# Optimization experiments

Hardware: AMD Instinct MI355X
Metric: run time of the kernel (lower is better)

Reference implementation:

```python
import jax, jax.numpy as jnp
import numpy as np

D_MODEL = 1024
NHEAD = 16
HEAD_DIM = D_MODEL // NHEAD
B, S = 8, 1024
NEG = -1e9  # finite stand-in for -inf (same softmax result, grad-safe)


def setup_inputs() -> dict:
    key = jax.random.key(0)
    ks = jax.random.split(key, 12)
    sc = 1.0 / np.sqrt(D_MODEL)
    inp = {
        "q": jax.random.normal(ks[0], (B, S, D_MODEL), jnp.float32),
        "k": jax.random.normal(ks[1], (B, S, D_MODEL), jnp.float32),
        "v": jax.random.normal(ks[2], (B, S, D_MODEL), jnp.float32),
        "padding_mask": jax.random.bernoulli(ks[3], 0.1, (B, S)),
        "causal_mask": jnp.where(jnp.tril(jnp.ones((S, S), bool)), 0.0, NEG).astype(jnp.float32),
        "wq": jax.random.normal(ks[4], (D_MODEL, D_MODEL), jnp.float32) * sc,
        "bq": jax.random.normal(ks[5], (D_MODEL,), jnp.float32) * sc,
        "wk": jax.random.normal(ks[6], (D_MODEL, D_MODEL), jnp.float32) * sc,
        "wv": jax.random.normal(ks[7], (D_MODEL, D_MODEL), jnp.float32) * sc,
        "bv": jax.random.normal(ks[8], (D_MODEL,), jnp.float32) * sc,
        "wo": jax.random.normal(ks[9], (D_MODEL, D_MODEL), jnp.float32) * sc,
        "bo": jax.random.normal(ks[10], (D_MODEL,), jnp.float32) * sc,
    }
    return inp


def reference(q, k, v, padding_mask, causal_mask, wq, bq, wk, wv, bv, wo, bo):
    b = q.shape[0]
    # projections (torch Linear: x @ W.T + b); k_linear has no bias
    qp = q @ wq.T + bq
    kp = k @ wk.T
    vp = v @ wv.T + bv
    # [B, S, H, Dh] -> [B, H, S, Dh]
    qh = qp.reshape(b, -1, NHEAD, HEAD_DIM).transpose(0, 2, 1, 3)
    kh = kp.reshape(b, -1, NHEAD, HEAD_DIM).transpose(0, 2, 1, 3)
    vh = vp.reshape(b, -1, NHEAD, HEAD_DIM).transpose(0, 2, 1, 3)
    scores = jnp.einsum("bhqd,bhkd->bhqk", qh, kh) / np.sqrt(HEAD_DIM).astype(np.float32)
    scores = jnp.where(padding_mask[:, None, None, :], NEG, scores)
    scores = scores + causal_mask[None, None, :, :]
    attn = jax.nn.softmax(scores, axis=-1)
    out = jnp.einsum("bhqk,bhkd->bhqd", attn, vh)
    out = out.transpose(0, 2, 1, 3).reshape(b, -1, D_MODEL)
    return out @ wo.T + bo
```

## Files before the change

### kernel.cpp

```cpp
#include <hip/hip_runtime.h>
#include <hip/hip_bf16.h>
#include <cstdint>
#include <math.h>


typedef __bf16 bf16_t;
typedef __bf16 bf16x8 __attribute__((ext_vector_type(8)));
typedef __bf16 bf16x4 __attribute__((ext_vector_type(4)));
typedef float  f32x4  __attribute__((ext_vector_type(4)));

#define MFMA16(a, b, c) __builtin_amdgcn_mfma_f32_16x16x32_bf16((a), (b), (c), 0, 0, 0)
#define NEGV (-1e9f)

__device__ __forceinline__ void gl_lds16(const void* gp, void* lp) {
  __builtin_amdgcn_global_load_lds(
      (__attribute__((address_space(1))) void*)(gp),
      (__attribute__((address_space(3))) void*)(lp), 16, 0, 0);
}

__device__ __forceinline__ unsigned int pk2(float lo, float hi) {
  unsigned short a = __builtin_bit_cast(unsigned short, (bf16_t)lo);
  unsigned short b = __builtin_bit_cast(unsigned short, (bf16_t)hi);
  return (unsigned int)a | ((unsigned int)b << 16);
}

__device__ __forceinline__ void cvt_body(const float* __restrict__ in,
                                         bf16_t* __restrict__ out, int i) {
  const float4* p = reinterpret_cast<const float4*>(in) + (size_t)i * 2;
  float4 a = p[0], b = p[1];
  bf16x8 r = {(bf16_t)a.x, (bf16_t)a.y, (bf16_t)a.z, (bf16_t)a.w,
              (bf16_t)b.x, (bf16_t)b.y, (bf16_t)b.z, (bf16_t)b.w};
  *reinterpret_cast<bf16x8*>(out + (size_t)i * 8) = r;
}

__global__ __launch_bounds__(256) void cvt_all(
    const float* __restrict__ q, const float* __restrict__ k, const float* __restrict__ v,
    const float* __restrict__ wq, const float* __restrict__ wk,
    const float* __restrict__ wv, const float* __restrict__ wo,
    bf16_t* __restrict__ oq, bf16_t* __restrict__ ok, bf16_t* __restrict__ ov,
    bf16_t* __restrict__ owq, bf16_t* __restrict__ owk,
    bf16_t* __restrict__ owv, bf16_t* __restrict__ owo) {
  const int bid = (int)blockIdx.x;
  if (bid < 12288) {
    const int s = bid >> 12;
    const int i = (bid & 4095) * 256 + (int)threadIdx.x;
    cvt_body(s == 0 ? q : (s == 1 ? k : v),
             s == 0 ? oq : (s == 1 ? ok : ov), i);
  } else {
    const int r = bid - 12288;
    const int s = r >> 9;
    const int i = (r & 511) * 256 + (int)threadIdx.x;
    cvt_body(s == 0 ? wq : (s == 1 ? wk : (s == 2 ? wv : wo)),
             s == 0 ? owq : (s == 1 ? owk : (s == 2 ? owv : owo)), i);
  }
}

__device__ __forceinline__ void panel_decode(int r, int& bx, int& by) {
  const int t8 = r >> 3;
  bx = t8 & 7;
  by = ((t8 >> 3) << 3) | (r & 7);
}

__global__ __launch_bounds__(256) void gemm_qkv(const bf16_t* __restrict__ qbf,
                                                const bf16_t* __restrict__ kbf,
                                                const bf16_t* __restrict__ vbf,
                                                const bf16_t* __restrict__ wqb,
                                                const bf16_t* __restrict__ wkb,
                                                const bf16_t* __restrict__ wvb,
                                                const float* __restrict__ bq,
                                                const float* __restrict__ bv,
                                                bf16_t* __restrict__ qp,
                                                bf16_t* __restrict__ kp,
                                                bf16_t* __restrict__ vtw) {
  __shared__ bf16_t smem[6][128 * 32];
  const int z = blockIdx.y;
  const bf16_t* A = z == 0 ? qbf : (z == 1 ? kbf : vbf);
  const bf16_t* W = z == 0 ? wqb : (z == 1 ? wkb : wvb);
  const int t = threadIdx.x;
  const int w = t >> 6, l = t & 63, lr = l & 15, lg = l >> 4;
  int bx, by;
  panel_decode((int)blockIdx.x, bx, by);
  const int m0 = by * 128, n0 = bx * 128;
  const int wm = (w >> 1) * 64, wn = (w & 1) * 64;
  const int K = 1024, N = 1024;

  f32x4 acc[4][4] = {};
  const int swsrc = ((t & 3) ^ ((t >> 3) & 3)) * 8;
  const bf16_t* Ag = A + (size_t)(m0 + (t >> 2)) * K + swsrc;
  const bf16_t* Wg = W + (size_t)(n0 + (t >> 2)) * K + swsrc;

  auto stage = [&](int buf, int tile) {
    const int kt = tile * 32;
    gl_lds16(Ag + kt,                  (char*)(smem[buf])     + t * 16);
    gl_lds16(Ag + kt + (size_t)64 * K, (char*)(smem[buf])     + 4096 + t * 16);
    gl_lds16(Wg + kt,                  (char*)(smem[3 + buf]) + t * 16);
    gl_lds16(Wg + kt + (size_t)64 * K, (char*)(smem[3 + buf]) + 4096 + t * 16);
  };

  stage(0, 0);
  stage(1, 1);

  const int cofs = ((lg ^ ((lr >> 1) & 3)) << 4);
  for (int it = 0; it < 32; ++it) {
    if (it < 31) asm volatile("s_waitcnt vmcnt(4)" ::: "memory");
    else         asm volatile("s_waitcnt vmcnt(0)" ::: "memory");
    __builtin_amdgcn_s_barrier();
    if (it + 2 < 32) stage((it + 2) % 3, it + 2);

    const char* AsB = (const char*)(smem[it % 3]);
    const char* BsB = (const char*)(smem[3 + it % 3]);
    bf16x8 af[4], bfr[4];
#pragma unroll
    for (int mt = 0; mt < 4; mt++)
      af[mt] = *reinterpret_cast<const bf16x8*>(AsB + (wm + mt * 16 + lr) * 64 + cofs);
#pragma unroll
    for (int nt = 0; nt < 4; nt++)
      bfr[nt] = *reinterpret_cast<const bf16x8*>(BsB + (wn + nt * 16 + lr) * 64 + cofs);
#pragma unroll
    for (int mt = 0; mt < 4; mt++)
#pragma unroll
      for (int nt = 0; nt < 4; nt++)
        acc[mt][nt] = MFMA16(af[mt], bfr[nt], acc[mt][nt]);
  }

  if (z != 2) {
    bf16_t* outp = (z == 0) ? qp : kp;
    const float sc = (z == 0) ? 0.125f : 1.0f;
#pragma unroll
    for (int nt = 0; nt < 4; nt++) {
      const int col = n0 + wn + nt * 16 + lr;
      const float bb = (z == 0) ? bq[col] : 0.0f;
#pragma unroll
      for (int mt = 0; mt < 4; mt++)
#pragma unroll
        for (int i = 0; i < 4; i++) {
          const int row = m0 + wm + mt * 16 + lg * 4 + i;
          outp[(size_t)row * N + col] = (bf16_t)((acc[mt][nt][i] + bb) * sc);
        }
    }
  } else {
    __syncthreads();
    char* T = (char*)smem;
#pragma unroll
    for (int nt = 0; nt < 4; nt++) {
      const int col_l = wn + nt * 16 + lr;
      const float bb = bv[n0 + col_l];
#pragma unroll
      for (int mt = 0; mt < 4; mt++)
#pragma unroll
        for (int i = 0; i < 4; i++) {
          const int row_l = wm + mt * 16 + lg * 4 + i;
          *(bf16_t*)(T + col_l * 256 + ((row_l * 2) ^ ((col_l & 7) << 4))) =
              (bf16_t)(acc[mt][nt][i] + bb);
        }
    }
    __syncthreads();
    const int b = m0 >> 10, s0 = m0 & 1023;
    const int c_l = t >> 1, half = t & 1;
    bf16_t* dst = vtw + (size_t)(b * 1024 + n0 + c_l) * 1024 + s0 + half * 64;
    const char* Trow = T + c_l * 256;
    const int sw = c_l & 7;
#pragma unroll
    for (int jj = 0; jj < 8; jj++) {
      const int lc = half * 8 + jj;
      bf16x8 vv = *reinterpret_cast<const bf16x8*>(Trow + ((lc ^ sw) << 4));
      *reinterpret_cast<bf16x8*>(dst + jj * 8) = vv;
    }
  }
}

__global__ __launch_bounds__(256) void gemm_out(const bf16_t* __restrict__ A,
                                                const bf16_t* __restrict__ W,
                                                const float* __restrict__ bias,
                                                float* __restrict__ outp) {
  __shared__ bf16_t smem[6][128 * 32];
  const int t = threadIdx.x;
  const int w = t >> 6, l = t & 63, lr = l & 15, lg = l >> 4;
  int bx, by;
  panel_decode((int)blockIdx.x, bx, by);
  const int m0 = by * 128, n0 = bx * 128;
  const int wm = (w >> 1) * 64, wn = (w & 1) * 64;
  const int K = 1024, N = 1024;

  f32x4 acc[4][4] = {};
  const int swsrc = ((t & 3) ^ ((t >> 3) & 3)) * 8;
  const bf16_t* Ag = A + (size_t)(m0 + (t >> 2)) * K + swsrc;
  const bf16_t* Wg = W + (size_t)(n0 + (t >> 2)) * K + swsrc;

  auto stage = [&](int buf, int tile) {
    const int kt = tile * 32;
    gl_lds16(Ag + kt,                  (char*)(smem[buf])     + t * 16);
    gl_lds16(Ag + kt + (size_t)64 * K, (char*)(smem[buf])     + 4096 + t * 16);
    gl_lds16(Wg + kt,                  (char*)(smem[3 + buf]) + t * 16);
    gl_lds16(Wg + kt + (size_t)64 * K, (char*)(smem[3 + buf]) + 4096 + t * 16);
  };

  stage(0, 0);
  stage(1, 1);

  const int cofs = ((lg ^ ((lr >> 1) & 3)) << 4);
  for (int it = 0; it < 32; ++it) {
    if (it < 31) asm volatile("s_waitcnt vmcnt(4)" ::: "memory");
    else         asm volatile("s_waitcnt vmcnt(0)" ::: "memory");
    __builtin_amdgcn_s_barrier();
    if (it + 2 < 32) stage((it + 2) % 3, it + 2);

    const char* AsB = (const char*)(smem[it % 3]);
    const char* BsB = (const char*)(smem[3 + it % 3]);
    bf16x8 af[4], bfr[4];
#pragma unroll
    for (int mt = 0; mt < 4; mt++)
      af[mt] = *reinterpret_cast<const bf16x8*>(AsB + (wm + mt * 16 + lr) * 64 + cofs);
#pragma unroll
    for (int nt = 0; nt < 4; nt++)
      bfr[nt] = *reinterpret_cast<const bf16x8*>(BsB + (wn + nt * 16 + lr) * 64 + cofs);
#pragma unroll
    for (int mt = 0; mt < 4; mt++)
#pragma unroll
      for (int nt = 0; nt < 4; nt++)
        acc[mt][nt] = MFMA16(af[mt], bfr[nt], acc[mt][nt]);
  }

#pragma unroll
  for (int nt = 0; nt < 4; nt++) {
    const int col = n0 + wn + nt * 16 + lr;
    const float bb = bias[col];
#pragma unroll
    for (int mt = 0; mt < 4; mt++)
#pragma unroll
      for (int i = 0; i < 4; i++) {
        const int row = m0 + wm + mt * 16 + lg * 4 + i;
        outp[(size_t)row * N + col] = acc[mt][nt][i] + bb;
      }
  }
}

__device__ __forceinline__ void pack_bfly(const f32x4 (&s)[4], int lg,
                                          bf16x8& pbv0, bf16x8& pbv1) {
  unsigned int u[4][2], sh[4][2];
#pragma unroll
  for (int nt = 0; nt < 4; nt++) {
    u[nt][0] = pk2(s[nt][0], s[nt][1]);
    u[nt][1] = pk2(s[nt][2], s[nt][3]);
  }
#pragma unroll
  for (int nt = 0; nt < 4; nt++) {
    sh[nt][0] = (unsigned int)__shfl_xor((int)u[nt][0], 16, 64);
    sh[nt][1] = (unsigned int)__shfl_xor((int)u[nt][1], 16, 64);
  }
  const bool ev = (lg & 1) == 0;
  unsigned int Y[8];
  Y[0] = ev ? u[0][0] : sh[1][0];  Y[1] = ev ? u[0][1] : sh[1][1];
  Y[2] = ev ? u[2][0] : sh[3][0];  Y[3] = ev ? u[2][1] : sh[3][1];
  Y[4] = ev ? sh[0][0] : u[1][0];  Y[5] = ev ? sh[0][1] : u[1][1];
  Y[6] = ev ? sh[2][0] : u[3][0];  Y[7] = ev ? sh[2][1] : u[3][1];
  const bool mid = (lg == 1) || (lg == 2);
#pragma unroll
  for (int j = 0; j < 8; j++) {
    const unsigned int z = (unsigned int)__shfl_xor((int)Y[j], 48, 64);
    Y[j] = mid ? z : Y[j];
  }
  union U8 { unsigned int u[4]; bf16x8 v; };
  U8 p0, p1;
  p0.u[0] = Y[0]; p0.u[1] = Y[1]; p0.u[2] = Y[4]; p0.u[3] = Y[5];
  p1.u[0] = Y[2]; p1.u[1] = Y[3]; p1.u[2] = Y[6]; p1.u[3] = Y[7];
  pbv0 = p0.v;
  pbv1 = p1.v;
}

__global__ __launch_bounds__(512, 8) void attn_fused(const bf16_t* __restrict__ qp,
                                                     const bf16_t* __restrict__ kp,
                                                     const bf16_t* __restrict__ vt,
                                                     const int* __restrict__ pad,
                                                     bf16_t* __restrict__ outp) {
  __shared__ bf16_t Ks[2][64 * 64];
  __shared__ bf16_t Vts[2][64 * 64];
  __shared__ int padI[1024];
  __shared__ int sfl[8], sfh[8];
  const int t = threadIdx.x, w = t >> 6, l = t & 63, lr = l & 15, lg = l >> 4;
  const int L = (int)blockIdx.x;
  const int bh = (L & 7) + ((L >> 6) << 3);
  const int j = (L >> 3) & 7;
  const int b = bh >> 4, h = bh & 15;
  const int lo = j, hi = 15 - j;

  const int srow = t >> 3, sc = t & 7;
  const int gc = sc ^ (srow & 7);
  const bf16_t* kgb = kp + (size_t)(b * 1024 + srow) * 1024 + h * 64 + gc * 8;
  const bf16_t* vgb = vt + (size_t)(bh * 64 + srow) * 1024 + gc * 8;

  auto stage = [&](int bufi, int k0s) {
    gl_lds16(kgb + (size_t)k0s * 1024, (char*)(Ks[bufi]) + t * 16);
    gl_lds16(vgb + k0s,                (char*)(Vts[bufi]) + t * 16);
  };

  bool unl = false, unh = false;
  for (int jj = t; jj <= hi * 64; jj += 512) {
    const bool u = (pad[b * 1024 + jj] == 0);
    unh |= u;
    unl |= (u && (jj <= lo * 64));
  }
  const bool al = __any(unl), ah = __any(unh);
  if (l == 0) { sfl[w] = al ? 1 : 0; sfh[w] = ah ? 1 : 0; }

  stage(0, 0);
  if (t < 256) gl_lds16(pad + b * 1024 + t * 4, (char*)padI + t * 16);

  const int mytile = (w < 4) ? hi : lo;
  const int qrow_l = mytile * 64 + (w & 3) * 16 + lr;
  const int base16 = mytile * 64 + (w & 3) * 16;
  const bf16_t* qg = qp + (size_t)(b * 1024 + qrow_l) * 1024 + h * 64 + lg * 8;
  const bf16x8 qa0 = *reinterpret_cast<const bf16x8*>(qg);
  const bf16x8 qa1 = *reinterpret_cast<const bf16x8*>(qg + 32);

  __syncthreads();
  int ul = 0, uh = 0;
#pragma unroll
  for (int i = 0; i < 8; i++) { ul |= sfl[i]; uh |= sfh[i]; }
  const bool mydeg = (w < 4) ? (uh == 0) : (ul == 0);
  const int ktEnd = (ul == 0) ? 16 : (hi + 1);

  f32x4 o[4] = {};
  float m_ = -INFINITY, ld_ = 0.0f;

  for (int kt = 0; kt < ktEnd; ++kt) {
    const int cur = kt & 1;
    if (kt + 1 < ktEnd) {
      stage(cur ^ 1, (kt + 1) * 64);
      asm volatile("s_waitcnt vmcnt(2)" ::: "memory");
    } else {
      asm volatile("s_waitcnt vmcnt(0)" ::: "memory");
    }
    __builtin_amdgcn_s_barrier();

    if (kt <= mytile || mydeg) {
      const char* Kb = (const char*)(Ks[cur]);
      const char* Vb = (const char*)(Vts[cur]);
      const int k0 = kt * 64;

      f32x4 s[4] = {};
#pragma unroll
      for (int nt = 0; nt < 4; nt++) {
        const int row = nt * 16 + lr;
        const int sw = (row & 7) << 4;
        bf16x8 kb0 = *reinterpret_cast<const bf16x8*>(Kb + row * 128 + ((lg * 16) ^ sw));
        bf16x8 kb1 = *reinterpret_cast<const bf16x8*>(Kb + row * 128 + ((lg * 16 + 64) ^ sw));
        s[nt] = MFMA16(kb0, qa0, s[nt]);
        s[nt] = MFMA16(kb1, qa1, s[nt]);
      }

      const bool nc = (k0 + 63 > base16);
#pragma unroll
      for (int nt = 0; nt < 4; nt++) {
        const int kc4 = k0 + nt * 16 + lg * 4;
        const int4 pd = *reinterpret_cast<const int4*>(&padI[kc4]);
        const int pdv[4] = {pd.x, pd.y, pd.z, pd.w};
#pragma unroll
        for (int i = 0; i < 4; i++) {
          float v = s[nt][i];
          if (pdv[i]) v = NEGV;
          if (nc && (kc4 + i > qrow_l)) v += NEGV;
          s[nt][i] = v;
        }
      }

      float mx = s[0][0];
#pragma unroll
      for (int nt = 0; nt < 4; nt++)
#pragma unroll
        for (int i = 0; i < 4; i++) mx = fmaxf(mx, s[nt][i]);
      mx = fmaxf(mx, __shfl_xor(mx, 16, 64));
      mx = fmaxf(mx, __shfl_xor(mx, 32, 64));

      if (!__all(mx <= m_ - 88.0f)) {
        if (!__all(mx <= m_ + 8.0f)) {
          const float mn = fmaxf(m_, mx);
          const float scl = __expf(m_ - mn);
          m_ = mn;
          ld_ *= scl;
#pragma unroll
          for (int nt = 0; nt < 4; nt++) o[nt] *= scl;
        }
        float a = 0.0f;
#pragma unroll
        for (int nt = 0; nt < 4; nt++)
#pragma unroll
          for (int i = 0; i < 4; i++) {
            const float p = __expf(s[nt][i] - m_);
            s[nt][i] = p;
            a += p;
          }
        a += __shfl_xor(a, 16, 64);
        a += __shfl_xor(a, 32, 64);
        ld_ += a;

        bf16x8 pb0, pb1;
        pack_bfly(s, lg, pb0, pb1);

#pragma unroll
        for (int nt = 0; nt < 4; nt++) {
          const int vrow = nt * 16 + lr;
          const int vsw = (vrow & 7) << 4;
          bf16x8 vf0 = *reinterpret_cast<const bf16x8*>(Vb + vrow * 128 + ((lg * 16) ^ vsw));
          bf16x8 vf1 = *reinterpret_cast<const bf16x8*>(Vb + vrow * 128 + ((64 + lg * 16) ^ vsw));
          o[nt] = MFMA16(vf0, pb0, o[nt]);
          o[nt] = MFMA16(vf1, pb1, o[nt]);
        }
      }
    }
    __builtin_amdgcn_s_barrier();
  }

  const float rinv = 1.0f / ld_;
#pragma unroll
  for (int nt = 0; nt < 4; nt++) {
    bf16x4 r = {(bf16_t)(o[nt][0] * rinv), (bf16_t)(o[nt][1] * rinv),
                (bf16_t)(o[nt][2] * rinv), (bf16_t)(o[nt][3] * rinv)};
    *reinterpret_cast<bf16x4*>(outp + (size_t)(b * 1024 + qrow_l) * 1024 + h * 64 + nt * 16 + lg * 4) = r;
  }
}

extern "C" void kernel_launch(void* const* d_in, const int* in_sizes, int n_in,
                              void* d_out, int out_size, void* d_ws, size_t ws_size,
                              hipStream_t stream) {
  const float* q   = (const float*)d_in[0];
  const float* k   = (const float*)d_in[1];
  const float* v   = (const float*)d_in[2];
  const int*   pad = (const int*)d_in[3];
  const float* wq  = (const float*)d_in[5];
  const float* bq  = (const float*)d_in[6];
  const float* wk  = (const float*)d_in[7];
  const float* wv  = (const float*)d_in[8];
  const float* bv  = (const float*)d_in[9];
  const float* wo  = (const float*)d_in[10];
  const float* bo  = (const float*)d_in[11];

  char* ws = (char*)d_ws;
  const size_t MiB = 1024 * 1024;
  bf16_t* qbf = (bf16_t*)(ws + 0 * MiB);
  bf16_t* kbf = (bf16_t*)(ws + 16 * MiB);
  bf16_t* vbf = (bf16_t*)(ws + 32 * MiB);
  bf16_t* qp  = (bf16_t*)(ws + 48 * MiB);
  bf16_t* kp  = (bf16_t*)(ws + 64 * MiB);
  bf16_t* vtw = (bf16_t*)(ws + 80 * MiB);
  bf16_t* wqb = (bf16_t*)(ws + 96 * MiB);
  bf16_t* wkb = (bf16_t*)(ws + 98 * MiB);
  bf16_t* wvb = (bf16_t*)(ws + 100 * MiB);
  bf16_t* wob = (bf16_t*)(ws + 102 * MiB);
  bf16_t* attnO = qbf;

  cvt_all<<<14336, 256, 0, stream>>>(q, k, v, wq, wk, wv, wo,
                                     qbf, kbf, vbf, wqb, wkb, wvb, wob);

  gemm_qkv<<<dim3(512, 3), 256, 0, stream>>>(qbf, kbf, vbf, wqb, wkb, wvb, bq, bv, qp, kp, vtw);

  attn_fused<<<1024, 512, 0, stream>>>(qp, kp, vtw, pad, attnO);

  gemm_out<<<512, 256, 0, stream>>>(attnO, wob, bo, (float*)d_out);
}
```

Before: 187.4 us.

## Rewrite QKV projection GEMM with 256x256 tiles and 8-wave ping-pong pipeline

```diff
diff --git a/kernel.cpp b/kernel.cpp
--- a/kernel.cpp
+++ b/kernel.cpp
@@ -16,6 +16,12 @@
   __builtin_amdgcn_global_load_lds(
       (__attribute__((address_space(1))) void*)(gp),
       (__attribute__((address_space(3))) void*)(lp), 16, 0, 0);
+}
+
+__device__ __forceinline__ void bar() {
+  asm volatile("" ::: "memory");
+  __builtin_amdgcn_s_barrier();
+  asm volatile("" ::: "memory");
 }
 
 __device__ __forceinline__ unsigned int pk2(float lo, float hi) {
@@ -55,13 +61,7 @@
   }
 }
 
-__device__ __forceinline__ void panel_decode(int r, int& bx, int& by) {
-  const int t8 = r >> 3;
-  bx = t8 & 7;
-  by = ((t8 >> 3) << 3) | (r & 7);
-}
-
-__global__ __launch_bounds__(256) void gemm_qkv(const bf16_t* __restrict__ qbf,
+__global__ __launch_bounds__(512) void gemm_qkv(const bf16_t* __restrict__ qbf,
                                                 const bf16_t* __restrict__ kbf,
                                                 const bf16_t* __restrict__ vbf,
                                                 const bf16_t* __restrict__ wqb,
@@ -72,55 +72,128 @@
                                                 bf16_t* __restrict__ qp,
                                                 bf16_t* __restrict__ kp,
                                                 bf16_t* __restrict__ vtw) {
-  __shared__ bf16_t smem[6][128 * 32];
-  const int z = blockIdx.y;
+  __shared__ __align__(16) char lds[131072];
+  const int bid = (int)blockIdx.x;
+  const int z = bid >> 7;
+  const int r = bid & 127;
+  const int p = ((r >> 5) << 3) | (r & 7);
+  const int ntile = (r >> 3) & 3;
   const bf16_t* A = z == 0 ? qbf : (z == 1 ? kbf : vbf);
   const bf16_t* W = z == 0 ? wqb : (z == 1 ? wkb : wvb);
   const int t = threadIdx.x;
   const int w = t >> 6, l = t & 63, lr = l & 15, lg = l >> 4;
-  int bx, by;
-  panel_decode((int)blockIdx.x, bx, by);
-  const int m0 = by * 128, n0 = bx * 128;
-  const int wm = (w >> 1) * 64, wn = (w & 1) * 64;
+  const int wr = w >> 2, wc = w & 3;
+  const int m0 = p * 256, n0 = ntile * 256;
   const int K = 1024, N = 1024;
 
-  f32x4 acc[4][4] = {};
-  const int swsrc = ((t & 3) ^ ((t >> 3) & 3)) * 8;
-  const bf16_t* Ag = A + (size_t)(m0 + (t >> 2)) * K + swsrc;
-  const bf16_t* Wg = W + (size_t)(n0 + (t >> 2)) * K + swsrc;
-
-  auto stage = [&](int buf, int tile) {
-    const int kt = tile * 32;
-    gl_lds16(Ag + kt,                  (char*)(smem[buf])     + t * 16);
-    gl_lds16(Ag + kt + (size_t)64 * K, (char*)(smem[buf])     + 4096 + t * 16);
-    gl_lds16(Wg + kt,                  (char*)(smem[3 + buf]) + t * 16);
-    gl_lds16(Wg + kt + (size_t)64 * K, (char*)(smem[3 + buf]) + 4096 + t * 16);
+  const int gc = (t & 7) ^ ((t >> 3) & 7);
+  const bf16_t* Ag = A + (size_t)(m0 + (t >> 3)) * K + gc * 8;
+  const bf16_t* Wg = W + (size_t)(n0 + (t >> 3)) * K + gc * 8;
+
+  auto stageA = [&](int buf, int tile, int half) {
+    char* dst = lds + buf * 65536 + half * 16384 + t * 16;
+    const size_t kt = (size_t)tile * 64;
+    gl_lds16(Ag + (size_t)(half * 128) * K + kt,      dst);
+    gl_lds16(Ag + (size_t)(half * 128 + 64) * K + kt, dst + 8192);
   };
-
-  stage(0, 0);
-  stage(1, 1);
-
-  const int cofs = ((lg ^ ((lr >> 1) & 3)) << 4);
-  for (int it = 0; it < 32; ++it) {
-    if (it < 31) asm volatile("s_waitcnt vmcnt(4)" ::: "memory");
-    else         asm volatile("s_waitcnt vmcnt(0)" ::: "memory");
-    __builtin_amdgcn_s_barrier();
-    if (it + 2 < 32) stage((it + 2) % 3, it + 2);
-
-    const char* AsB = (const char*)(smem[it % 3]);
-    const char* BsB = (const char*)(smem[3 + it % 3]);
-    bf16x8 af[4], bfr[4];
-#pragma unroll
-    for (int mt = 0; mt < 4; mt++)
-      af[mt] = *reinterpret_cast<const bf16x8*>(AsB + (wm + mt * 16 + lr) * 64 + cofs);
-#pragma unroll
-    for (int nt = 0; nt < 4; nt++)
-      bfr[nt] = *reinterpret_cast<const bf16x8*>(BsB + (wn + nt * 16 + lr) * 64 + cofs);
-#pragma unroll
-    for (int mt = 0; mt < 4; mt++)
-#pragma unroll
-      for (int nt = 0; nt < 4; nt++)
-        acc[mt][nt] = MFMA16(af[mt], bfr[nt], acc[mt][nt]);
+  auto stageB = [&](int buf, int tile, int half) {
+    char* dst = lds + buf * 65536 + 32768 + half * 16384 + t * 16;
+    const size_t kt = (size_t)tile * 64;
+    gl_lds16(Wg + (size_t)(half * 128) * K + kt,      dst);
+    gl_lds16(Wg + (size_t)(half * 128 + 64) * K + kt, dst + 8192);
+  };
+
+  stageA(0, 0, 0); stageA(0, 0, 1); stageB(0, 0, 0); stageB(0, 0, 1);
+  stageB(1, 1, 0); stageB(1, 1, 1); stageA(1, 1, 0);
+  asm volatile("s_waitcnt vmcnt(6)" ::: "memory");
+  bar();
+
+  f32x4 acc[8][4] = {};
+  const int xorv = (lr & 7) << 4;
+  const int k0o = lg * 16, k1o = 64 + lg * 16;
+
+  for (int T = 0; T < 16; ++T) {
+    const int cur = T & 1;
+    const char* Ab = lds + cur * 65536;
+    const char* Bb = Ab + 32768;
+
+    bf16x8 a0[4][2], a1[4][2], b0[2][2], b1[2][2];
+#pragma unroll
+    for (int mt = 0; mt < 4; mt++) {
+      const int row = wr * 128 + mt * 16 + lr;
+      a0[mt][0] = *(const bf16x8*)(Ab + row * 128 + (k0o ^ xorv));
+      a0[mt][1] = *(const bf16x8*)(Ab + row * 128 + (k1o ^ xorv));
+    }
+#pragma unroll
+    for (int nt = 0; nt < 2; nt++) {
+      const int row = wc * 64 + nt * 16 + lr;
+      b0[nt][0] = *(const bf16x8*)(Bb + row * 128 + (k0o ^ xorv));
+      b0[nt][1] = *(const bf16x8*)(Bb + row * 128 + (k1o ^ xorv));
+    }
+    if (T + 1 < 16) stageA(cur ^ 1, T + 1, 1);
+    bar();
+    asm volatile("s_waitcnt lgkmcnt(0)" ::: "memory");
+    __builtin_amdgcn_s_setprio(1);
+#pragma unroll
+    for (int mt = 0; mt < 4; mt++)
+#pragma unroll
+      for (int nt = 0; nt < 2; nt++) {
+        acc[mt][nt] = MFMA16(a0[mt][0], b0[nt][0], acc[mt][nt]);
+        acc[mt][nt] = MFMA16(a0[mt][1], b0[nt][1], acc[mt][nt]);
+      }
+    __builtin_amdgcn_s_setprio(0);
+    bar();
+#pragma unroll
+    for (int nt = 0; nt < 2; nt++) {
+      const int row = wc * 64 + (nt + 2) * 16 + lr;
+      b1[nt][0] = *(const bf16x8*)(Bb + row * 128 + (k0o ^ xorv));
+      b1[nt][1] = *(const bf16x8*)(Bb + row * 128 + (k1o ^ xorv));
+    }
+    bar();
+    asm volatile("s_waitcnt lgkmcnt(0)" ::: "memory");
+    __builtin_amdgcn_s_setprio(1);
+#pragma unroll
+    for (int mt = 0; mt < 4; mt++)
+#pragma unroll
+      for (int nt = 0; nt < 2; nt++) {
+        acc[mt][nt + 2] = MFMA16(a0[mt][0], b1[nt][0], acc[mt][nt + 2]);
+        acc[mt][nt + 2] = MFMA16(a0[mt][1], b1[nt][1], acc[mt][nt + 2]);
+      }
+    __builtin_amdgcn_s_setprio(0);
+    bar();
+#pragma unroll
+    for (int mt = 0; mt < 4; mt++) {
+      const int row = wr * 128 + (mt + 4) * 16 + lr;
+      a1[mt][0] = *(const bf16x8*)(Ab + row * 128 + (k0o ^ xorv));
+      a1[mt][1] = *(const bf16x8*)(Ab + row * 128 + (k1o ^ xorv));
+    }
+    if (T + 2 < 16) stageB(cur, T + 2, 0);
+    bar();
+    asm volatile("s_waitcnt lgkmcnt(0)" ::: "memory");
+    __builtin_amdgcn_s_setprio(1);
+#pragma unroll
+    for (int mt = 0; mt < 4; mt++)
+#pragma unroll
+      for (int nt = 0; nt < 2; nt++) {
+        acc[mt + 4][nt + 2] = MFMA16(a1[mt][0], b1[nt][0], acc[mt + 4][nt + 2]);
+        acc[mt + 4][nt + 2] = MFMA16(a1[mt][1], b1[nt][1], acc[mt + 4][nt + 2]);
+      }
+    __builtin_amdgcn_s_setprio(0);
+    bar();
+    if (T + 2 < 16) { stageB(cur, T + 2, 1); stageA(cur, T + 2, 0); }
+    if (T < 14)       asm volatile("s_waitcnt vmcnt(6)" ::: "memory");
+    else if (T == 14) asm volatile("s_waitcnt vmcnt(0)" ::: "memory");
+    bar();
+    __builtin_amdgcn_s_setprio(1);
+#pragma unroll
+    for (int mt = 0; mt < 4; mt++)
+#pragma unroll
+      for (int nt = 0; nt < 2; nt++) {
+        acc[mt + 4][nt] = MFMA16(a1[mt][0], b0[nt][0], acc[mt + 4][nt]);
+        acc[mt + 4][nt] = MFMA16(a1[mt][1], b0[nt][1], acc[mt + 4][nt]);
+      }
+    __builtin_amdgcn_s_setprio(0);
+    bar();
   }
 
   if (z != 2) {
@@ -128,45 +201,50 @@
     const float sc = (z == 0) ? 0.125f : 1.0f;
 #pragma unroll
     for (int nt = 0; nt < 4; nt++) {
-      const int col = n0 + wn + nt * 16 + lr;
+      const int col = n0 + wc * 64 + nt * 16 + lr;
       const float bb = (z == 0) ? bq[col] : 0.0f;
 #pragma unroll
-      for (int mt = 0; mt < 4; mt++)
+      for (int mt = 0; mt < 8; mt++)
 #pragma unroll
         for (int i = 0; i < 4; i++) {
-          const int row = m0 + wm + mt * 16 + lg * 4 + i;
+          const int row = m0 + wr * 128 + mt * 16 + lg * 4 + i;
           outp[(size_t)row * N + col] = (bf16_t)((acc[mt][nt][i] + bb) * sc);
         }
     }
   } else {
     __syncthreads();
-    char* T = (char*)smem;
+    char* Tl = lds;
 #pragma unroll
     for (int nt = 0; nt < 4; nt++) {
-      const int col_l = wn + nt * 16 + lr;
+      const int col_l = wc * 64 + nt * 16 + lr;
       const float bb = bv[n0 + col_l];
 #pragma unroll
-      for (int mt = 0; mt < 4; mt++)
+      for (int mt = 0; mt < 8; mt++)
 #pragma unroll
         for (int i = 0; i < 4; i++) {
-          const int row_l = wm + mt * 16 + lg * 4 + i;
-          *(bf16_t*)(T + col_l * 256 + ((row_l * 2) ^ ((col_l & 7) << 4))) =
+          const int row_l = wr * 128 + mt * 16 + lg * 4 + i;
+          *(bf16_t*)(Tl + col_l * 512 + ((row_l * 2) ^ ((col_l & 7) << 4))) =
               (bf16_t)(acc[mt][nt][i] + bb);
         }
     }
     __syncthreads();
     const int b = m0 >> 10, s0 = m0 & 1023;
-    const int c_l = t >> 1, half = t & 1;
-    bf16_t* dst = vtw + (size_t)(b * 1024 + n0 + c_l) * 1024 + s0 + half * 64;
-    const char* Trow = T + c_l * 256;
-    const int sw = c_l & 7;
-#pragma unroll
-    for (int jj = 0; jj < 8; jj++) {
-      const int lc = half * 8 + jj;
-      bf16x8 vv = *reinterpret_cast<const bf16x8*>(Trow + ((lc ^ sw) << 4));
-      *reinterpret_cast<bf16x8*>(dst + jj * 8) = vv;
-    }
-  }
+    const int c_l = t >> 1, hf = t & 1;
+    bf16_t* dst = vtw + (size_t)(b * 1024 + n0 + c_l) * 1024 + s0 + hf * 128;
+    const char* Trow = Tl + c_l * 512;
+    const int sw2 = (c_l & 7) << 4;
+#pragma unroll
+    for (int jj = 0; jj < 16; jj++) {
+      bf16x8 vv = *(const bf16x8*)(Trow + ((((hf * 16 + jj) << 4)) ^ sw2));
+      *(bf16x8*)(dst + jj * 8) = vv;
+    }
+  }
+}
+
+__device__ __forceinline__ void panel_decode(int r, int& bx, int& by) {
+  const int t8 = r >> 3;
+  bx = t8 & 7;
+  by = ((t8 >> 3) << 3) | (r & 7);
 }
 
 __global__ __launch_bounds__(256) void gemm_out(const bf16_t* __restrict__ A,
@@ -187,8 +265,7 @@
   const bf16_t* Ag = A + (size_t)(m0 + (t >> 2)) * K + swsrc;
   const bf16_t* Wg = W + (size_t)(n0 + (t >> 2)) * K + swsrc;
 
-  auto stage = [&](int buf, int tile) {
-    const int kt = tile * 32;
+  auto stage = [&](int buf, int kt) {
     gl_lds16(Ag + kt,                  (char*)(smem[buf])     + t * 16);
     gl_lds16(Ag + kt + (size_t)64 * K, (char*)(smem[buf])     + 4096 + t * 16);
     gl_lds16(Wg + kt,                  (char*)(smem[3 + buf]) + t * 16);
@@ -196,14 +273,15 @@
   };
 
   stage(0, 0);
-  stage(1, 1);
+  stage(1, 32);
 
   const int cofs = ((lg ^ ((lr >> 1) & 3)) << 4);
   for (int it = 0; it < 32; ++it) {
     if (it < 31) asm volatile("s_waitcnt vmcnt(4)" ::: "memory");
     else         asm volatile("s_waitcnt vmcnt(0)" ::: "memory");
     __builtin_amdgcn_s_barrier();
-    if (it + 2 < 32) stage((it + 2) % 3, it + 2);
+    asm volatile("" ::: "memory");
+    if (it + 2 < 32) stage((it + 2) % 3, (it + 2) * 32);
 
     const char* AsB = (const char*)(smem[it % 3]);
     const char* BsB = (const char*)(smem[3 + it % 3]);
@@ -414,9 +492,9 @@
   const float rinv = 1.0f / ld_;
 #pragma unroll
   for (int nt = 0; nt < 4; nt++) {
-    bf16x4 r = {(bf16_t)(o[nt][0] * rinv), (bf16_t)(o[nt][1] * rinv),
-                (bf16_t)(o[nt][2] * rinv), (bf16_t)(o[nt][3] * rinv)};
-    *reinterpret_cast<bf16x4*>(outp + (size_t)(b * 1024 + qrow_l) * 1024 + h * 64 + nt * 16 + lg * 4) = r;
+    bf16x4 rr = {(bf16_t)(o[nt][0] * rinv), (bf16_t)(o[nt][1] * rinv),
+                 (bf16_t)(o[nt][2] * rinv), (bf16_t)(o[nt][3] * rinv)};
+    *reinterpret_cast<bf16x4*>(outp + (size_t)(b * 1024 + qrow_l) * 1024 + h * 64 + nt * 16 + lg * 4) = rr;
   }
 }
 
@@ -452,7 +530,7 @@
   cvt_all<<<14336, 256, 0, stream>>>(q, k, v, wq, wk, wv, wo,
                                      qbf, kbf, vbf, wqb, wkb, wvb, wob);
 
-  gemm_qkv<<<dim3(512, 3), 256, 0, stream>>>(qbf, kbf, vbf, wqb, wkb, wvb, bq, bv, qp, kp, vtw);
+  gemm_qkv<<<384, 512, 0, stream>>>(qbf, kbf, vbf, wqb, wkb, wvb, bq, bv, qp, kp, vtw);
 
   attn_fused<<<1024, 512, 0, stream>>>(qp, kp, vtw, pad, attnO);
 
```

Result: no change. 187.4 us (+0.0%).

## Restructure projection GEMMs to 256x128 tiles with 8 waves and split-phase pipeline

Applied to the files above, without the earlier changes.

```diff
diff --git a/kernel.cpp b/kernel.cpp
--- a/kernel.cpp
+++ b/kernel.cpp
@@ -16,6 +16,12 @@
   __builtin_amdgcn_global_load_lds(
       (__attribute__((address_space(1))) void*)(gp),
       (__attribute__((address_space(3))) void*)(lp), 16, 0, 0);
+}
+
+__device__ __forceinline__ void bar() {
+  asm volatile("" ::: "memory");
+  __builtin_amdgcn_s_barrier();
+  asm volatile("" ::: "memory");
 }
 
 __device__ __forceinline__ unsigned int pk2(float lo, float hi) {
@@ -55,13 +61,83 @@
   }
 }
 
-__device__ __forceinline__ void panel_decode(int r, int& bx, int& by) {
-  const int t8 = r >> 3;
-  bx = t8 & 7;
-  by = ((t8 >> 3) << 3) | (r & 7);
-}
-
-__global__ __launch_bounds__(256) void gemm_qkv(const bf16_t* __restrict__ qbf,
+
+#define GEMM_KLOOP(Ag, Wg, lds, acc, lr, lg, wr, wc)                          \
+  auto stageA = [&](int buf, int tile) {                                      \
+    char* dst = lds + buf * 32768 + t * 16;                                   \
+    const size_t kt = (size_t)tile * 64;                                      \
+    gl_lds16(Ag + kt,                    dst);                                \
+    gl_lds16(Ag + kt + (size_t)64 * K,   dst + 8192);                         \
+    gl_lds16(Ag + kt + (size_t)128 * K,  dst + 16384);                        \
+    gl_lds16(Ag + kt + (size_t)192 * K,  dst + 24576);                        \
+  };                                                                          \
+  auto stageB = [&](int buf, int tile) {                                      \
+    char* dst = lds + 98304 + buf * 16384 + t * 16;                           \
+    const size_t kt = (size_t)tile * 64;                                      \
+    gl_lds16(Wg + kt,                    dst);                                \
+    gl_lds16(Wg + kt + (size_t)64 * K,   dst + 8192);                         \
+  };                                                                          \
+  stageA(0, 0); stageB(0, 0); stageA(1, 1); stageB(1, 1);                     \
+  asm volatile("s_waitcnt vmcnt(6)" ::: "memory");   \
+  bar();                                                      \
+  const int xorv = (lr & 7) << 4;                                             \
+  const int k0o = lg * 16, k1o = 64 + lg * 16;                                \
+  for (int T = 0; T < 16; ++T) {                                              \
+    const int cur = T % 3;                                                    \
+    const char* Ab = lds + cur * 32768;                                       \
+    const char* Bb = lds + 98304 + cur * 16384;                               \
+    bf16x8 af[4][2], b0[2][2], b1[2][2];                                      \
+                                \
+    _Pragma("unroll")                                                         \
+    for (int mt = 0; mt < 4; mt++) {                                          \
+      const int row = wr * 64 + mt * 16 + lr;                                 \
+      af[mt][0] = *(const bf16x8*)(Ab + row * 128 + (k0o ^ xorv));            \
+      af[mt][1] = *(const bf16x8*)(Ab + row * 128 + (k1o ^ xorv));            \
+    }                                                                         \
+    _Pragma("unroll")                                                         \
+    for (int nt = 0; nt < 2; nt++) {                                          \
+      const int row = wc * 64 + nt * 16 + lr;                                 \
+      b0[nt][0] = *(const bf16x8*)(Bb + row * 128 + (k0o ^ xorv));            \
+      b0[nt][1] = *(const bf16x8*)(Bb + row * 128 + (k1o ^ xorv));            \
+    }                                                                         \
+    if (T + 2 < 16) stageA((T + 2) % 3, T + 2);                               \
+    bar();                                                                    \
+    asm volatile("s_waitcnt lgkmcnt(0)" ::: "memory");                        \
+    __builtin_amdgcn_s_setprio(1);                                            \
+    _Pragma("unroll")                                                         \
+    for (int mt = 0; mt < 4; mt++)                                            \
+      _Pragma("unroll")                                                       \
+      for (int nt = 0; nt < 2; nt++) {                                        \
+        acc[mt][nt] = MFMA16(af[mt][0], b0[nt][0], acc[mt][nt]);              \
+        acc[mt][nt] = MFMA16(af[mt][1], b0[nt][1], acc[mt][nt]);              \
+      }                                                                       \
+    __builtin_amdgcn_s_setprio(0);                                            \
+    bar();                                                                    \
+            \
+    _Pragma("unroll")                                                         \
+    for (int nt = 0; nt < 2; nt++) {                                          \
+      const int row = wc * 64 + (nt + 2) * 16 + lr;                           \
+      b1[nt][0] = *(const bf16x8*)(Bb + row * 128 + (k0o ^ xorv));            \
+      b1[nt][1] = *(const bf16x8*)(Bb + row * 128 + (k1o ^ xorv));            \
+    }                                                                         \
+    if (T + 2 < 16) stageB((T + 2) % 3, T + 2);                               \
+    if (T < 14)       asm volatile("s_waitcnt vmcnt(6)" ::: "memory");        \
+    else if (T == 14) asm volatile("s_waitcnt vmcnt(0)" ::: "memory");        \
+    bar();                                     \
+    asm volatile("s_waitcnt lgkmcnt(0)" ::: "memory");                        \
+    __builtin_amdgcn_s_setprio(1);                                            \
+    _Pragma("unroll")                                                         \
+    for (int mt = 0; mt < 4; mt++)                                            \
+      _Pragma("unroll")                                                       \
+      for (int nt = 0; nt < 2; nt++) {                                        \
+        acc[mt][nt + 2] = MFMA16(af[mt][0], b1[nt][0], acc[mt][nt + 2]);      \
+        acc[mt][nt + 2] = MFMA16(af[mt][1], b1[nt][1], acc[mt][nt + 2]);      \
+      }                                                                       \
+    __builtin_amdgcn_s_setprio(0);                                            \
+    bar();                                                                    \
+  }
+
+__global__ __launch_bounds__(512) void gemm_qkv(const bf16_t* __restrict__ qbf,
                                                 const bf16_t* __restrict__ kbf,
                                                 const bf16_t* __restrict__ vbf,
                                                 const bf16_t* __restrict__ wqb,
@@ -72,164 +148,103 @@
                                                 bf16_t* __restrict__ qp,
                                                 bf16_t* __restrict__ kp,
                                                 bf16_t* __restrict__ vtw) {
-  __shared__ bf16_t smem[6][128 * 32];
-  const int z = blockIdx.y;
+  __shared__ __align__(16) char lds[147456];
+  const int bid = (int)blockIdx.x;
+  const int z = bid >> 8;
+  const int idx = bid & 255;
+  const int p = ((idx >> 6) << 3) | (idx & 7);
+  const int n = (idx >> 3) & 7;
   const bf16_t* A = z == 0 ? qbf : (z == 1 ? kbf : vbf);
   const bf16_t* W = z == 0 ? wqb : (z == 1 ? wkb : wvb);
   const int t = threadIdx.x;
   const int w = t >> 6, l = t & 63, lr = l & 15, lg = l >> 4;
-  int bx, by;
-  panel_decode((int)blockIdx.x, bx, by);
-  const int m0 = by * 128, n0 = bx * 128;
-  const int wm = (w >> 1) * 64, wn = (w & 1) * 64;
+  const int wr = w >> 1, wc = w & 1;
+  const int m0 = p * 256, n0 = n * 128;
   const int K = 1024, N = 1024;
 
+  const int gc = (t & 7) ^ ((t >> 3) & 7);
+  const bf16_t* Ag = A + (size_t)(m0 + (t >> 3)) * K + gc * 8;
+  const bf16_t* Wg = W + (size_t)(n0 + (t >> 3)) * K + gc * 8;
+
   f32x4 acc[4][4] = {};
-  const int swsrc = ((t & 3) ^ ((t >> 3) & 3)) * 8;
-  const bf16_t* Ag = A + (size_t)(m0 + (t >> 2)) * K + swsrc;
-  const bf16_t* Wg = W + (size_t)(n0 + (t >> 2)) * K + swsrc;
-
-  auto stage = [&](int buf, int tile) {
-    const int kt = tile * 32;
-    gl_lds16(Ag + kt,                  (char*)(smem[buf])     + t * 16);
-    gl_lds16(Ag + kt + (size_t)64 * K, (char*)(smem[buf])     + 4096 + t * 16);
-    gl_lds16(Wg + kt,                  (char*)(smem[3 + buf]) + t * 16);
-    gl_lds16(Wg + kt + (size_t)64 * K, (char*)(smem[3 + buf]) + 4096 + t * 16);
-  };
-
-  stage(0, 0);
-  stage(1, 1);
-
-  const int cofs = ((lg ^ ((lr >> 1) & 3)) << 4);
-  for (int it = 0; it < 32; ++it) {
-    if (it < 31) asm volatile("s_waitcnt vmcnt(4)" ::: "memory");
-    else         asm volatile("s_waitcnt vmcnt(0)" ::: "memory");
-    __builtin_amdgcn_s_barrier();
-    if (it + 2 < 32) stage((it + 2) % 3, it + 2);
-
-    const char* AsB = (const char*)(smem[it % 3]);
-    const char* BsB = (const char*)(smem[3 + it % 3]);
-    bf16x8 af[4], bfr[4];
-#pragma unroll
-    for (int mt = 0; mt < 4; mt++)
-      af[mt] = *reinterpret_cast<const bf16x8*>(AsB + (wm + mt * 16 + lr) * 64 + cofs);
-#pragma unroll
-    for (int nt = 0; nt < 4; nt++)
-      bfr[nt] = *reinterpret_cast<const bf16x8*>(BsB + (wn + nt * 16 + lr) * 64 + cofs);
-#pragma unroll
-    for (int mt = 0; mt < 4; mt++)
-#pragma unroll
-      for (int nt = 0; nt < 4; nt++)
-        acc[mt][nt] = MFMA16(af[mt], bfr[nt], acc[mt][nt]);
-  }
+  GEMM_KLOOP(Ag, Wg, lds, acc, lr, lg, wr, wc)
 
   if (z != 2) {
     bf16_t* outp = (z == 0) ? qp : kp;
     const float sc = (z == 0) ? 0.125f : 1.0f;
 #pragma unroll
     for (int nt = 0; nt < 4; nt++) {
-      const int col = n0 + wn + nt * 16 + lr;
+      const int col = n0 + wc * 64 + nt * 16 + lr;
       const float bb = (z == 0) ? bq[col] : 0.0f;
 #pragma unroll
       for (int mt = 0; mt < 4; mt++)
 #pragma unroll
         for (int i = 0; i < 4; i++) {
-          const int row = m0 + wm + mt * 16 + lg * 4 + i;
+          const int row = m0 + wr * 64 + mt * 16 + lg * 4 + i;
           outp[(size_t)row * N + col] = (bf16_t)((acc[mt][nt][i] + bb) * sc);
         }
     }
   } else {
     __syncthreads();
-    char* T = (char*)smem;
+    char* Tl = lds;
 #pragma unroll
     for (int nt = 0; nt < 4; nt++) {
-      const int col_l = wn + nt * 16 + lr;
+      const int col_l = wc * 64 + nt * 16 + lr;
       const float bb = bv[n0 + col_l];
 #pragma unroll
       for (int mt = 0; mt < 4; mt++)
 #pragma unroll
         for (int i = 0; i < 4; i++) {
-          const int row_l = wm + mt * 16 + lg * 4 + i;
-          *(bf16_t*)(T + col_l * 256 + ((row_l * 2) ^ ((col_l & 7) << 4))) =
+          const int row_l = wr * 64 + mt * 16 + lg * 4 + i;
+          *(bf16_t*)(Tl + col_l * 512 + ((row_l * 2) ^ ((col_l & 7) << 4))) =
               (bf16_t)(acc[mt][nt][i] + bb);
         }
     }
     __syncthreads();
     const int b = m0 >> 10, s0 = m0 & 1023;
-    const int c_l = t >> 1, half = t & 1;
-    bf16_t* dst = vtw + (size_t)(b * 1024 + n0 + c_l) * 1024 + s0 + half * 64;
-    const char* Trow = T + c_l * 256;
-    const int sw = c_l & 7;
+    const int c_l = t >> 2, sub = t & 3;
+    bf16_t* dst = vtw + (size_t)(b * 1024 + n0 + c_l) * 1024 + s0 + sub * 64;
+    const char* Trow = Tl + c_l * 512;
+    const int sw2 = (c_l & 7) << 4;
 #pragma unroll
     for (int jj = 0; jj < 8; jj++) {
-      const int lc = half * 8 + jj;
-      bf16x8 vv = *reinterpret_cast<const bf16x8*>(Trow + ((lc ^ sw) << 4));
-      *reinterpret_cast<bf16x8*>(dst + jj * 8) = vv;
+      const int lc = sub * 8 + jj;
+      bf16x8 vv = *(const bf16x8*)(Trow + ((lc << 4) ^ sw2));
+      *(bf16x8*)(dst + jj * 8) = vv;
     }
   }
 }
 
-__global__ __launch_bounds__(256) void gemm_out(const bf16_t* __restrict__ A,
+__global__ __launch_bounds__(512) void gemm_out(const bf16_t* __restrict__ A,
                                                 const bf16_t* __restrict__ W,
                                                 const float* __restrict__ bias,
                                                 float* __restrict__ outp) {
-  __shared__ bf16_t smem[6][128 * 32];
+  __shared__ __align__(16) char lds[147456];
+  const int bid = (int)blockIdx.x;
+  const int p = ((bid >> 6) << 3) | (bid & 7);
+  const int n = (bid >> 3) & 7;
   const int t = threadIdx.x;
   const int w = t >> 6, l = t & 63, lr = l & 15, lg = l >> 4;
-  int bx, by;
-  panel_decode((int)blockIdx.x, bx, by);
-  const int m0 = by * 128, n0 = bx * 128;
-  const int wm = (w >> 1) * 64, wn = (w & 1) * 64;
+  const int wr = w >> 1, wc = w & 1;
+  const int m0 = p * 256, n0 = n * 128;
   const int K = 1024, N = 1024;
 
+  const int gc = (t & 7) ^ ((t >> 3) & 7);
+  const bf16_t* Ag = A + (size_t)(m0 + (t >> 3)) * K + gc * 8;
+  const bf16_t* Wg = W + (size_t)(n0 + (t >> 3)) * K + gc * 8;
+
   f32x4 acc[4][4] = {};
-  const int swsrc = ((t & 3) ^ ((t >> 3) & 3)) * 8;
-  const bf16_t* Ag = A + (size_t)(m0 + (t >> 2)) * K + swsrc;
-  const bf16_t* Wg = W + (size_t)(n0 + (t >> 2)) * K + swsrc;
-
-  auto stage = [&](int buf, int tile) {
-    const int kt = tile * 32;
-    gl_lds16(Ag + kt,                  (char*)(smem[buf])     + t * 16);
-    gl_lds16(Ag + kt + (size_t)64 * K, (char*)(smem[buf])     + 4096 + t * 16);
-    gl_lds16(Wg + kt,                  (char*)(smem[3 + buf]) + t * 16);
-    gl_lds16(Wg + kt + (size_t)64 * K, (char*)(smem[3 + buf]) + 4096 + t * 16);
-  };
-
-  stage(0, 0);
-  stage(1, 1);
-
-  const int cofs = ((lg ^ ((lr >> 1) & 3)) << 4);
-  for (int it = 0; it < 32; ++it) {
-    if (it < 31) asm volatile("s_waitcnt vmcnt(4)" ::: "memory");
-    else         asm volatile("s_waitcnt vmcnt(0)" ::: "memory");
-    __builtin_amdgcn_s_barrier();
-    if (it + 2 < 32) stage((it + 2) % 3, it + 2);
-
-    const char* AsB = (const char*)(smem[it % 3]);
-    const char* BsB = (const char*)(smem[3 + it % 3]);
-    bf16x8 af[4], bfr[4];
+  GEMM_KLOOP(Ag, Wg, lds, acc, lr, lg, wr, wc)
+
+#pragma unroll
+  for (int nt = 0; nt < 4; nt++) {
+    const int col = n0 + wc * 64 + nt * 16 + lr;
+    const float bb = bias[col];
 #pragma unroll
     for (int mt = 0; mt < 4; mt++)
-      af[mt] = *reinterpret_cast<const bf16x8*>(AsB + (wm + mt * 16 + lr) * 64 + cofs);
-#pragma unroll
-    for (int nt = 0; nt < 4; nt++)
-      bfr[nt] = *reinterpret_cast<const bf16x8*>(BsB + (wn + nt * 16 + lr) * 64 + cofs);
-#pragma unroll
-    for (int mt = 0; mt < 4; mt++)
-#pragma unroll
-      for (int nt = 0; nt < 4; nt++)
-        acc[mt][nt] = MFMA16(af[mt], bfr[nt], acc[mt][nt]);
-  }
-
-#pragma unroll
-  for (int nt = 0; nt < 4; nt++) {
-    const int col = n0 + wn + nt * 16 + lr;
-    const float bb = bias[col];
-#pragma unroll
-    for (int mt = 0; mt < 4; mt++)
 #pragma unroll
       for (int i = 0; i < 4; i++) {
-        const int row = m0 + wm + mt * 16 + lg * 4 + i;
+        const int row = m0 + wr * 64 + mt * 16 + lg * 4 + i;
         outp[(size_t)row * N + col] = acc[mt][nt][i] + bb;
       }
   }
@@ -414,9 +429,9 @@
   const float rinv = 1.0f / ld_;
 #pragma unroll
   for (int nt = 0; nt < 4; nt++) {
-    bf16x4 r = {(bf16_t)(o[nt][0] * rinv), (bf16_t)(o[nt][1] * rinv),
-                (bf16_t)(o[nt][2] * rinv), (bf16_t)(o[nt][3] * rinv)};
-    *reinterpret_cast<bf16x4*>(outp + (size_t)(b * 1024 + qrow_l) * 1024 + h * 64 + nt * 16 + lg * 4) = r;
+    bf16x4 rr = {(bf16_t)(o[nt][0] * rinv), (bf16_t)(o[nt][1] * rinv),
+                 (bf16_t)(o[nt][2] * rinv), (bf16_t)(o[nt][3] * rinv)};
+    *reinterpret_cast<bf16x4*>(outp + (size_t)(b * 1024 + qrow_l) * 1024 + h * 64 + nt * 16 + lg * 4) = rr;
   }
 }
 
@@ -452,9 +467,9 @@
   cvt_all<<<14336, 256, 0, stream>>>(q, k, v, wq, wk, wv, wo,
                                      qbf, kbf, vbf, wqb, wkb, wvb, wob);
 
-  gemm_qkv<<<dim3(512, 3), 256, 0, stream>>>(qbf, kbf, vbf, wqb, wkb, wvb, bq, bv, qp, kp, vtw);
+  gemm_qkv<<<768, 512, 0, stream>>>(qbf, kbf, vbf, wqb, wkb, wvb, bq, bv, qp, kp, vtw);
 
   attn_fused<<<1024, 512, 0, stream>>>(qp, kp, vtw, pad, attnO);
 
-  gemm_out<<<512, 256, 0, stream>>>(attnO, wob, bo, (float*)d_out);
-}
+  gemm_out<<<256, 512, 0, stream>>>(attnO, wob, bo, (float*)d_out);
+}
```

After: 174.1 us. 1.08x faster.
